# Kernel optimization log

Measured on AMD Instinct MI355X. Metric: run time of the kernel, lower is better.

The kernel has to match this reference:

```python
import jax, jax.numpy as jnp
import numpy as np

GRID_H, GRID_W = 14, 14  # grid_size from init_kwargs (crop_height, crop_width)


def _bilinear_crop(feature_map, boxes, bbox_idx, crop_h, crop_w):
    """crop_and_resize-style ROIAlign.

    feature_map: [N, C, H, W] float
    boxes:       [M, 4] (x1, y1, x2, y2) in feature-map pixel coords
    bbox_idx:    [M] int32 batch index per box
    returns:     [M, C, crop_h, crop_w]
    """
    N, C, H, W = feature_map.shape
    x1, y1, x2, y2 = boxes[:, 0], boxes[:, 1], boxes[:, 2], boxes[:, 3]

    # Sample points evenly spaced INCLUDING the box corners (tf.crop_and_resize grid).
    ti = jnp.arange(crop_h, dtype=boxes.dtype) / (crop_h - 1)  # [gh]
    tj = jnp.arange(crop_w, dtype=boxes.dtype) / (crop_w - 1)  # [gw]
    ys = y1[:, None] + (y2 - y1)[:, None] * ti  # [M, gh]
    xs = x1[:, None] + (x2 - x1)[:, None] * tj  # [M, gw]

    # Out-of-range samples get extrapolation value 0.
    my = (ys >= 0) & (ys <= H - 1)  # [M, gh]
    mx = (xs >= 0) & (xs <= W - 1)  # [M, gw]

    y0f = jnp.floor(ys)
    x0f = jnp.floor(xs)
    ly = ys - y0f  # [M, gh] lerp weights
    lx = xs - x0f  # [M, gw]

    y0 = jnp.clip(y0f, 0, H - 1).astype(jnp.int32)
    y1i = jnp.clip(y0f + 1, 0, H - 1).astype(jnp.int32)
    x0 = jnp.clip(x0f, 0, W - 1).astype(jnp.int32)
    x1i = jnp.clip(x0f + 1, 0, W - 1).astype(jnp.int32)

    b = bbox_idx[:, None, None]            # [M,1,1]
    Y0, Y1 = y0[:, :, None], y1i[:, :, None]   # [M,gh,1]
    X0, X1 = x0[:, None, :], x1i[:, None, :]   # [M,1,gw]

    # Advanced indexing with the channel slice in the middle -> result [M,gh,gw,C]
    g00 = feature_map[b, :, Y0, X0]
    g01 = feature_map[b, :, Y0, X1]
    g10 = feature_map[b, :, Y1, X0]
    g11 = feature_map[b, :, Y1, X1]

    wy = ly[:, :, None, None]  # [M,gh,1,1]
    wx = lx[:, None, :, None]  # [M,1,gw,1]
    out = (g00 * (1 - wy) * (1 - wx) + g01 * (1 - wy) * wx
           + g10 * wy * (1 - wx) + g11 * wy * wx)  # [M,gh,gw,C]

    mask = (my[:, :, None] & mx[:, None, :])[..., None]  # [M,gh,gw,1]
    out = jnp.where(mask, out, jnp.zeros((), out.dtype))
    return jnp.transpose(out, (0, 3, 1, 2))  # [M,C,gh,gw]


def setup_inputs() -> dict:
    key = jax.random.key(0)
    k1, k2, k3, k4, k5, k6, k7 = jax.random.split(key, 7)
    N, C, H, W = 4, 256, 200, 200
    img = 800  # original image height/width; stride = img / H = 4
    M = 2048

    feature_map = jax.random.normal(k1, (N, C, H, W), dtype=jnp.float32)

    n = jax.random.randint(k2, (M,), 0, N).astype(jnp.float32)
    score = jax.random.uniform(k3, (M,), dtype=jnp.float32)
    x1 = jax.random.uniform(k4, (M,), dtype=jnp.float32, maxval=img * 0.6)
    y1 = jax.random.uniform(k5, (M,), dtype=jnp.float32, maxval=img * 0.6)
    bw = jax.random.uniform(k6, (M,), dtype=jnp.float32, minval=16.0, maxval=img * 0.4)
    bh = jax.random.uniform(k7, (M,), dtype=jnp.float32, minval=16.0, maxval=img * 0.4)
    x2 = jnp.minimum(x1 + bw, img - 1.0)
    y2 = jnp.minimum(y1 + bh, img - 1.0)

    rois = jnp.stack([n, score, x1, y1, x2, y2], axis=1)  # [M, 6]
    return {"feature_map": feature_map, "rois": rois, "img_height": img}


def reference(feature_map, rois, img_height):
    H = feature_map.shape[2]
    stride = img_height / H
    bbox_idx = rois[:, 0].astype(jnp.int32)
    boxes = rois[:, 2:] / stride  # image coords -> feature-map coords
    return _bilinear_crop(feature_map, boxes, bbox_idx, GRID_H, GRID_W)
```

## Files before the change

kernel.cpp:

```cpp
#include <hip/hip_runtime.h>

#define GH 14
#define GW 14

__global__ __launch_bounds__(256) void roi_align_kernel(
    const float* __restrict__ fmap,
    const float* __restrict__ rois,
    const int*   __restrict__ imgh,
    float*       __restrict__ out,
    int C, int H, int W)
{
    const int per_box = C * GH * GW;
    const int m   = blockIdx.y;
    const int idx = blockIdx.x * blockDim.x + threadIdx.x;
    if (idx >= per_box) return;

    const int j = idx % GW;
    const int t = idx / GW;
    const int i = t % GH;
    const int c = t / GH;

    const float stride = (float)imgh[0] / (float)H;

    const float* r = rois + (size_t)m * 6;
    const int   b  = (int)r[0];
    const float x1 = r[2] / stride;
    const float y1 = r[3] / stride;
    const float x2 = r[4] / stride;
    const float y2 = r[5] / stride;

    const float ti = (float)i / (float)(GH - 1);
    const float tj = (float)j / (float)(GW - 1);
    const float ys = y1 + (y2 - y1) * ti;
    const float xs = x1 + (x2 - x1) * tj;

    const bool my = (ys >= 0.0f) && (ys <= (float)(H - 1));
    const bool mx = (xs >= 0.0f) && (xs <= (float)(W - 1));

    const float y0f = floorf(ys);
    const float x0f = floorf(xs);
    const float ly  = ys - y0f;
    const float lx  = xs - x0f;

    const int y0  = (int)fminf(fmaxf(y0f,        0.0f), (float)(H - 1));
    const int y1i = (int)fminf(fmaxf(y0f + 1.0f, 0.0f), (float)(H - 1));
    const int x0  = (int)fminf(fmaxf(x0f,        0.0f), (float)(W - 1));
    const int x1i = (int)fminf(fmaxf(x0f + 1.0f, 0.0f), (float)(W - 1));

    const float* p = fmap + ((size_t)b * C + c) * (size_t)(H * W);
    const float g00 = p[y0  * W + x0 ];
    const float g01 = p[y0  * W + x1i];
    const float g10 = p[y1i * W + x0 ];
    const float g11 = p[y1i * W + x1i];

    float v = g00 * (1.0f - ly) * (1.0f - lx)
            + g01 * (1.0f - ly) * lx
            + g10 * ly * (1.0f - lx)
            + g11 * ly * lx;
    v = (my && mx) ? v : 0.0f;

    out[(size_t)m * per_box + idx] = v;
}

extern "C" void kernel_launch(void* const* d_in, const int* in_sizes, int n_in,
                              void* d_out, int out_size, void* d_ws, size_t ws_size,
                              hipStream_t stream) {
    const float* fmap = (const float*)d_in[0];
    const float* rois = (const float*)d_in[1];
    const int*   imgh = (const int*)d_in[2];

    float* out = (float*)d_out;

    const int C = 256, H = 200, W = 200;
    const int M = in_sizes[1] / 6;
    const int per_box = C * GH * GW;
    const int blocks_x = (per_box + 255) / 256;

    dim3 grid(blocks_x, M);
    roi_align_kernel<<<grid, 256, 0, stream>>>(fmap, rois, imgh, out, C, H, W);
}
```

Before: 908.7 us.

## Loop over channel chunks per thread reusing precomputed bilinear indices and weights

Each block now handles one box and a chunk of 64 channels. Each thread owns one sample point, computes its offsets and mask-folded weights once, then loops over the channels in the chunk, striding by H*W. This removes the per-element index math and RoI loading that were repeated for every channel. The cost is that 60 of the 256 threads in each block sit idle, and there are fewer blocks in flight, which can lower occupancy and the loads in flight.

```diff
diff --git a/kernel.cpp b/kernel.cpp
--- a/kernel.cpp
+++ b/kernel.cpp
@@ -2,6 +2,7 @@
 
 #define GH 14
 #define GW 14
+#define CCHUNK 64
 
 __global__ __launch_bounds__(256) void roi_align_kernel(
     const float* __restrict__ fmap,
@@ -10,15 +11,14 @@
     float*       __restrict__ out,
     int C, int H, int W)
 {
-    const int per_box = C * GH * GW;
-    const int m   = blockIdx.y;
-    const int idx = blockIdx.x * blockDim.x + threadIdx.x;
-    if (idx >= per_box) return;
+    const int t = threadIdx.x;
+    if (t >= GH * GW) return;
 
-    const int j = idx % GW;
-    const int t = idx / GW;
-    const int i = t % GH;
-    const int c = t / GH;
+    const int m  = blockIdx.y;
+    const int c0 = blockIdx.x * CCHUNK;
+
+    const int j = t % GW;
+    const int i = t / GW;
 
     const float stride = (float)imgh[0] / (float)H;
 
@@ -47,19 +47,31 @@
     const int x0  = (int)fminf(fmaxf(x0f,        0.0f), (float)(W - 1));
     const int x1i = (int)fminf(fmaxf(x0f + 1.0f, 0.0f), (float)(W - 1));
 
-    const float* p = fmap + ((size_t)b * C + c) * (size_t)(H * W);
-    const float g00 = p[y0  * W + x0 ];
-    const float g01 = p[y0  * W + x1i];
-    const float g10 = p[y1i * W + x0 ];
-    const float g11 = p[y1i * W + x1i];
+    const float msk = (my && mx) ? 1.0f : 0.0f;
+    const float w00 = msk * (1.0f - ly) * (1.0f - lx);
+    const float w01 = msk * (1.0f - ly) * lx;
+    const float w10 = msk * ly * (1.0f - lx);
+    const float w11 = msk * ly * lx;
 
-    float v = g00 * (1.0f - ly) * (1.0f - lx)
-            + g01 * (1.0f - ly) * lx
-            + g10 * ly * (1.0f - lx)
-            + g11 * ly * lx;
-    v = (my && mx) ? v : 0.0f;
+    const int o00 = y0  * W + x0;
+    const int o01 = y0  * W + x1i;
+    const int o10 = y1i * W + x0;
+    const int o11 = y1i * W + x1i;
 
-    out[(size_t)m * per_box + idx] = v;
+    const int HW = H * W;
+    const float* __restrict__ p = fmap + ((size_t)b * C + c0) * (size_t)HW;
+    float*       __restrict__ o = out  + ((size_t)m * C + c0) * (size_t)(GH * GW) + t;
+
+    #pragma unroll 4
+    for (int c = 0; c < CCHUNK; ++c) {
+        const float g00 = p[o00];
+        const float g01 = p[o01];
+        const float g10 = p[o10];
+        const float g11 = p[o11];
+        *o = g00 * w00 + g01 * w01 + g10 * w10 + g11 * w11;
+        p += HW;
+        o += GH * GW;
+    }
 }
 
 extern "C" void kernel_launch(void* const* d_in, const int* in_sizes, int n_in,
@@ -73,9 +85,7 @@
 
     const int C = 256, H = 200, W = 200;
     const int M = in_sizes[1] / 6;
-    const int per_box = C * GH * GW;
-    const int blocks_x = (per_box + 255) / 256;
 
-    dim3 grid(blocks_x, M);
+    dim3 grid(C / CCHUNK, M);
     roi_align_kernel<<<grid, 256, 0, stream>>>(fmap, rois, imgh, out, C, H, W);
 }
```

Measured after the change: 912.2 us. No clear change (+0.4%).
